# Performance work log

Measured on AMD Instinct MI355X. Metric: run time of the kernel, lower is better.

The kernel has to match this reference:

```python
import jax, jax.numpy as jnp
import numpy as np

B, IN, OUT = 4, 32, 64
N, NS = 163842, 40962  # icosahedron mesh levels: NS = (N + 6) / 4
EPS = 1e-5
SLOPE = 0.2


def setup_inputs() -> dict:
    key = jax.random.key(0)
    ks = jax.random.split(key, 8)
    x = jax.random.normal(ks[0], (B, IN, N), dtype=jnp.float32)
    x1 = jax.random.normal(ks[1], (B, OUT, NS), dtype=jnp.float32)
    pool_neigh = jax.random.randint(ks[2], (NS * 7,), 0, N, dtype=jnp.int32)
    neigh = jax.random.randint(ks[3], (NS * 7,), 0, NS, dtype=jnp.int32)
    W1 = jax.random.normal(ks[4], (OUT, 7 * IN), dtype=jnp.float32) / np.sqrt(7 * IN).astype(np.float32)
    b1 = jnp.zeros((OUT,), dtype=jnp.float32)
    gamma = jnp.ones((OUT,), dtype=jnp.float32)
    beta = jnp.zeros((OUT,), dtype=jnp.float32)
    Wc = jax.random.normal(ks[5], (OUT, 2 * OUT), dtype=jnp.float32) / np.sqrt(2 * OUT).astype(np.float32)
    bc = jnp.zeros((OUT,), dtype=jnp.float32)
    return dict(x=x, x1=x1, pool_neigh=pool_neigh, neigh=neigh,
                W1=W1, b1=b1, gamma=gamma, beta=beta, Wc=Wc, bc=bc)


def reference(x, x1, pool_neigh, neigh, W1, b1, gamma, beta, Wc, bc):
    b, c, n = x.shape
    ns = (n + 6) // 4
    # pool_layer_batch ('mean'): gather 7-neighborhood on fine mesh, mean-pool
    pooled = x[:, :, pool_neigh[: ns * 7]].reshape(b, c, ns, 7).mean(axis=3)  # [B, IN, NS]
    # onering_conv_layer_batch: gather 7-stencil, reshape to [B, NS, 7*IN], linear
    mat = pooled[:, :, neigh].reshape(b, c, ns, 7)          # [B, IN, NS, 7]
    mat = mat.transpose(0, 2, 3, 1).reshape(b, ns, 7 * c)   # [B, NS, 7*IN]
    h = jnp.einsum('bnk,ok->bon', mat, W1) + b1[None, :, None]  # [B, OUT, NS]
    # BatchNorm1d (track_running_stats=False -> always batch stats) + LeakyReLU(0.2)
    mu = h.mean(axis=(0, 2), keepdims=True)
    var = h.var(axis=(0, 2), keepdims=True)
    h = gamma[None, :, None] * (h - mu) * jax.lax.rsqrt(var + EPS) + beta[None, :, None]
    h = jnp.where(h >= 0, h, SLOPE * h)
    # concat skip + 1x1 Conv1d
    cat = jnp.concatenate([h, x1], axis=1)                  # [B, 2*OUT, NS]
    out = jnp.einsum('bcn,oc->bon', cat, Wc) + bc[None, :, None]
    return out
```

## Files before the change

### kernel.cpp

```cpp
#include <hip/hip_runtime.h>
#include <cstddef>

#define NB    4
#define CIN   32
#define COUT  64
#define NFINE 163842
#define NSV   40962
#define EPSB  1e-5f
#define SLOPE 0.2f

typedef __attribute__((ext_vector_type(8))) short short8;
typedef __attribute__((ext_vector_type(4))) float f32x4;

#define O_XT   ((size_t)0)
#define O_H    ((size_t)0)
#define O_X1T  ((size_t)22 << 20)
#define O_POOL ((size_t)48 << 20)
#define O_W1F  ((size_t)60 << 20)
#define O_WCF  ((size_t)60 << 20 | 0x8000)
#define O_ST   ((size_t)61 << 20)

static __device__ __forceinline__ short f2bf(float f) {
    union { float f; unsigned u; } v; v.f = f;
    unsigned r = v.u + 0x7fffu + ((v.u >> 16) & 1u);
    return (short)(r >> 16);
}
static __device__ __forceinline__ float bf2f(short h) {
    union { unsigned u; float f; } v;
    v.u = ((unsigned)(unsigned short)h) << 16;
    return v.f;
}

__global__ void k_prep(const float* __restrict__ W1, const float* __restrict__ Wc,
                       short* __restrict__ W1f, short* __restrict__ Wcf,
                       float* __restrict__ stats) {
    if (threadIdx.x < 128) stats[threadIdx.x] = 0.f;
    for (int i = threadIdx.x; i < 7 * 4 * 64 * 8; i += 256) {
        int e = i & 7, l = (i >> 3) & 63, nf = (i >> 9) & 3, kk = i >> 11;
        int o = 16 * nf + (l & 15);
        int k = 32 * kk + 8 * (l >> 4) + e;
        W1f[i] = f2bf(W1[o * (7 * CIN) + k]);
    }
    for (int i = threadIdx.x; i < 4 * 4 * 64 * 8; i += 256) {
        int e = i & 7, l = (i >> 3) & 63, nf = (i >> 9) & 3, kk = i >> 11;
        int o = 16 * nf + (l & 15);
        int c = 32 * kk + 8 * (l >> 4) + e;
        Wcf[i] = f2bf(Wc[o * (2 * COUT) + c]);
    }
}

__global__ __launch_bounds__(256) void k_transpose(
        const float* __restrict__ x, short* __restrict__ xt) {
    __shared__ float tile[128][33];
    const int n0 = blockIdx.x * 128;
    const int b  = blockIdx.y;
    const float* xb = x + (size_t)b * CIN * NFINE;
#pragma unroll
    for (int q = 0; q < 16; ++q) {
        int i = threadIdx.x + 256 * q;
        int c = i >> 7, nl = i & 127;
        int n = n0 + nl;
        tile[nl][c] = (n < NFINE) ? xb[(size_t)c * NFINE + n] : 0.f;
    }
    __syncthreads();
#pragma unroll
    for (int q = 0; q < 2; ++q) {
        int i = threadIdx.x + 256 * q;
        int nl = i >> 2, cg = i & 3;
        int n = n0 + nl;
        if (n >= NFINE) continue;
        short8 o;
#pragma unroll
        for (int e = 0; e < 8; ++e) o[e] = f2bf(tile[nl][8 * cg + e]);
        *(short8*)(xt + ((size_t)b * NFINE + n) * CIN + 8 * cg) = o;
    }
}

__global__ __launch_bounds__(256) void k_x1t(
        const float* __restrict__ x1, short* __restrict__ x1t) {
    __shared__ float tile[64][68];
    const int s0 = blockIdx.x * 64;
    const int b  = blockIdx.y;
    const float* xb = x1 + (size_t)b * COUT * NSV;
#pragma unroll
    for (int q = 0; q < 16; ++q) {
        int i = threadIdx.x + 256 * q;
        int c = i >> 6, sl = i & 63;
        int s = s0 + sl;
        tile[sl][c] = (s < NSV) ? xb[(size_t)c * NSV + s] : 0.f;
    }
    __syncthreads();
#pragma unroll
    for (int q = 0; q < 2; ++q) {
        int i = threadIdx.x + 256 * q;
        int sl = i >> 3, cg = i & 7;
        int s = s0 + sl;
        if (s >= NSV) continue;
        short8 o;
#pragma unroll
        for (int e = 0; e < 8; ++e) o[e] = f2bf(tile[sl][8 * cg + e]);
        *(short8*)(x1t + ((size_t)b * NSV + s) * COUT + 8 * cg) = o;
    }
}

__global__ __launch_bounds__(256) void k_pool(
        const short* __restrict__ xt, const int* __restrict__ pn,
        short* __restrict__ pooled) {
    const int s = blockIdx.x * 256 + threadIdx.x;
    const int b = blockIdx.y;
    if (s >= NSV) return;
    float acc[CIN];
#pragma unroll
    for (int c = 0; c < CIN; ++c) acc[c] = 0.f;
#pragma unroll
    for (int j = 0; j < 7; ++j) {
        const int t = pn[7 * s + j];
        const short8* vp = (const short8*)(xt + ((size_t)b * NFINE + t) * CIN);
#pragma unroll
        for (int g = 0; g < 4; ++g) {
            short8 v = vp[g];
#pragma unroll
            for (int e = 0; e < 8; ++e) acc[8 * g + e] += bf2f(v[e]);
        }
    }
    short* op = pooled + ((size_t)b * NSV + s) * CIN;
#pragma unroll
    for (int g = 0; g < 4; ++g) {
        short8 o;
#pragma unroll
        for (int e = 0; e < 8; ++e) o[e] = f2bf(acc[8 * g + e] * (1.f / 7.f));
        *(short8*)(op + 8 * g) = o;
    }
}

__global__ __launch_bounds__(256) void k_conv(
        const int* __restrict__ neigh, const short* __restrict__ W1f,
        const short* __restrict__ pooled, short* __restrict__ hbf,
        float* __restrict__ stats) {
    __shared__ float red[2][4][COUT];
    const int l = threadIdx.x & 63, w = threadIdx.x >> 6;
    const int b = blockIdx.y;
    const int s0 = blockIdx.x * 128 + w * 32;
    const int r = l & 15, g = l >> 4;

    f32x4 acc[2][4];
#pragma unroll
    for (int mf = 0; mf < 2; ++mf)
#pragma unroll
        for (int nf = 0; nf < 4; ++nf) acc[mf][nf] = (f32x4){0.f, 0.f, 0.f, 0.f};

    const short* pb = pooled + (size_t)b * NSV * CIN;
    const int sA0 = s0 + r, sA1 = s0 + 16 + r;
    const bool v0 = sA0 < NSV, v1 = sA1 < NSV;

#pragma unroll
    for (int kk = 0; kk < 7; ++kk) {
        const int t0 = v0 ? neigh[7 * sA0 + kk] : 0;
        const int t1 = v1 ? neigh[7 * sA1 + kk] : 0;
        short8 a0 = *(const short8*)(pb + (size_t)t0 * CIN + 8 * g);
        short8 a1 = *(const short8*)(pb + (size_t)t1 * CIN + 8 * g);
        const short8* wf = (const short8*)(W1f) + (size_t)kk * 4 * 64;
        short8 b0 = wf[0 * 64 + l];
        short8 b1 = wf[1 * 64 + l];
        short8 b2 = wf[2 * 64 + l];
        short8 b3 = wf[3 * 64 + l];
        acc[0][0] = __builtin_amdgcn_mfma_f32_16x16x32_bf16(a0, b0, acc[0][0], 0, 0, 0);
        acc[0][1] = __builtin_amdgcn_mfma_f32_16x16x32_bf16(a0, b1, acc[0][1], 0, 0, 0);
        acc[0][2] = __builtin_amdgcn_mfma_f32_16x16x32_bf16(a0, b2, acc[0][2], 0, 0, 0);
        acc[0][3] = __builtin_amdgcn_mfma_f32_16x16x32_bf16(a0, b3, acc[0][3], 0, 0, 0);
        acc[1][0] = __builtin_amdgcn_mfma_f32_16x16x32_bf16(a1, b0, acc[1][0], 0, 0, 0);
        acc[1][1] = __builtin_amdgcn_mfma_f32_16x16x32_bf16(a1, b1, acc[1][1], 0, 0, 0);
        acc[1][2] = __builtin_amdgcn_mfma_f32_16x16x32_bf16(a1, b2, acc[1][2], 0, 0, 0);
        acc[1][3] = __builtin_amdgcn_mfma_f32_16x16x32_bf16(a1, b3, acc[1][3], 0, 0, 0);
    }

    float sum[4], sq[4];
#pragma unroll
    for (int nf = 0; nf < 4; ++nf) { sum[nf] = 0.f; sq[nf] = 0.f; }
#pragma unroll
    for (int mf = 0; mf < 2; ++mf)
#pragma unroll
        for (int nf = 0; nf < 4; ++nf) {
            f32x4 d = acc[mf][nf];
#pragma unroll
            for (int rr = 0; rr < 4; ++rr) {
                const int srow = s0 + 16 * mf + 4 * g + rr;
                const float v = d[rr];
                const bool ok = srow < NSV;
                if (ok) hbf[((size_t)b * NSV + srow) * COUT + 16 * nf + r] = f2bf(v);
                const float vm = ok ? v : 0.f;
                sum[nf] += vm; sq[nf] += vm * vm;
            }
        }
#pragma unroll
    for (int nf = 0; nf < 4; ++nf) {
        float a = sum[nf], c = sq[nf];
        a += __shfl_xor(a, 16); a += __shfl_xor(a, 32);
        c += __shfl_xor(c, 16); c += __shfl_xor(c, 32);
        if (g == 0) { red[0][w][16 * nf + r] = a; red[1][w][16 * nf + r] = c; }
    }
    __syncthreads();
    if (threadIdx.x < COUT) {
        const int o = threadIdx.x;
        atomicAdd(&stats[o],        red[0][0][o] + red[0][1][o] + red[0][2][o] + red[0][3][o]);
        atomicAdd(&stats[COUT + o], red[1][0][o] + red[1][1][o] + red[1][2][o] + red[1][3][o]);
    }
}

__global__ void k_stats(const float* __restrict__ gamma,
                        const float* __restrict__ beta, float* __restrict__ st) {
    const int o = threadIdx.x;
    const float cnt = (float)((size_t)NB * NSV);
    float mu  = st[o] / cnt;
    float var = st[COUT + o] / cnt - mu * mu;
    float sc  = gamma[o] * rsqrtf(var + EPSB);
    st[2 * COUT + o] = sc;
    st[3 * COUT + o] = beta[o] - mu * sc;
}

__global__ __launch_bounds__(256) void k_out(
        const short* __restrict__ hbf, const short* __restrict__ x1t,
        const short* __restrict__ Wcf, const float* __restrict__ st,
        const float* __restrict__ bc, float* __restrict__ out) {
    __shared__ __attribute__((aligned(16))) short Wcs[4 * 4 * 64 * 8];
    __shared__ float scs[COUT], shs[COUT], bcs[COUT];
    {
        const short8* src = (const short8*)Wcf;
        short8* dst = (short8*)Wcs;
        for (int i = threadIdx.x; i < 1024; i += 256) dst[i] = src[i];
        if (threadIdx.x < COUT) {
            scs[threadIdx.x] = st[2 * COUT + threadIdx.x];
            shs[threadIdx.x] = st[3 * COUT + threadIdx.x];
            bcs[threadIdx.x] = bc[threadIdx.x];
        }
    }
    __syncthreads();

    const int l = threadIdx.x & 63, w = threadIdx.x >> 6;
    const int b = blockIdx.y;
    const int s0 = blockIdx.x * 128 + w * 32;
    const int r = l & 15, g = l >> 4;

    float scv[16], shv[16];
#pragma unroll
    for (int kk = 0; kk < 2; ++kk)
#pragma unroll
        for (int e = 0; e < 8; ++e) {
            scv[8 * kk + e] = scs[32 * kk + 8 * g + e];
            shv[8 * kk + e] = shs[32 * kk + 8 * g + e];
        }

    f32x4 acc[2][4];
#pragma unroll
    for (int mf = 0; mf < 2; ++mf)
#pragma unroll
        for (int nf = 0; nf < 4; ++nf) acc[mf][nf] = (f32x4){0.f, 0.f, 0.f, 0.f};

    int sa0 = s0 + r;       if (sa0 > NSV - 1) sa0 = NSV - 1;
    int sa1 = s0 + 16 + r;  if (sa1 > NSV - 1) sa1 = NSV - 1;
    const size_t rowA0 = ((size_t)b * NSV + sa0) * COUT;
    const size_t rowA1 = ((size_t)b * NSV + sa1) * COUT;

#pragma unroll
    for (int kk = 0; kk < 4; ++kk) {
        short8 a0, a1;
        if (kk < 2) {
            short8 h0 = *(const short8*)(hbf + rowA0 + 32 * kk + 8 * g);
            short8 h1 = *(const short8*)(hbf + rowA1 + 32 * kk + 8 * g);
#pragma unroll
            for (int e = 0; e < 8; ++e) {
                float z0 = scv[8 * kk + e] * bf2f(h0[e]) + shv[8 * kk + e];
                float z1 = scv[8 * kk + e] * bf2f(h1[e]) + shv[8 * kk + e];
                z0 = fmaxf(z0, SLOPE * z0);
                z1 = fmaxf(z1, SLOPE * z1);
                a0[e] = f2bf(z0); a1[e] = f2bf(z1);
            }
        } else {
            a0 = *(const short8*)(x1t + rowA0 + 32 * (kk - 2) + 8 * g);
            a1 = *(const short8*)(x1t + rowA1 + 32 * (kk - 2) + 8 * g);
        }
        const short8* wf = (const short8*)Wcs + kk * 4 * 64;
#pragma unroll
        for (int nf = 0; nf < 4; ++nf) {
            short8 bfv = wf[nf * 64 + l];
            acc[0][nf] = __builtin_amdgcn_mfma_f32_16x16x32_bf16(a0, bfv, acc[0][nf], 0, 0, 0);
            acc[1][nf] = __builtin_amdgcn_mfma_f32_16x16x32_bf16(a1, bfv, acc[1][nf], 0, 0, 0);
        }
    }

    float* ob = out + (size_t)b * COUT * NSV;
#pragma unroll
    for (int mf = 0; mf < 2; ++mf)
#pragma unroll
        for (int nf = 0; nf < 4; ++nf) {
            const int o  = 16 * nf + r;
            const int sr = s0 + 16 * mf + 4 * g;
            f32x4 d = acc[mf][nf];
            const float bb = bcs[o];
            float* p = ob + (size_t)o * NSV + sr;
            if (sr + 3 < NSV) {
                *(float2*)(p)     = make_float2(d[0] + bb, d[1] + bb);
                *(float2*)(p + 2) = make_float2(d[2] + bb, d[3] + bb);
            } else {
#pragma unroll
                for (int rr = 0; rr < 4; ++rr)
                    if (sr + rr < NSV) p[rr] = d[rr] + bb;
            }
        }
}

extern "C" void kernel_launch(void* const* d_in, const int* in_sizes, int n_in,
                              void* d_out, int out_size, void* d_ws, size_t ws_size,
                              hipStream_t stream) {
    const float* x          = (const float*)d_in[0];
    const float* x1         = (const float*)d_in[1];
    const int*   pool_neigh = (const int*)d_in[2];
    const int*   neigh      = (const int*)d_in[3];
    const float* W1         = (const float*)d_in[4];
    const float* gamma      = (const float*)d_in[6];
    const float* beta       = (const float*)d_in[7];
    const float* Wc         = (const float*)d_in[8];
    const float* bc         = (const float*)d_in[9];

    char* wsb = (char*)d_ws;
    short* xt     = (short*)(wsb + O_XT);
    short* hbf    = (short*)(wsb + O_H);
    short* x1t    = (short*)(wsb + O_X1T);
    short* pooled = (short*)(wsb + O_POOL);
    short* W1f    = (short*)(wsb + O_W1F);
    short* Wcf    = (short*)(wsb + O_WCF);
    float* stats  = (float*)(wsb + O_ST);
    float* out    = (float*)d_out;

    k_prep<<<1, 256, 0, stream>>>(W1, Wc, W1f, Wcf, stats);
    k_transpose<<<dim3((NFINE + 127) / 128, NB), 256, 0, stream>>>(x, xt);
    k_pool<<<dim3((NSV + 255) / 256, NB), 256, 0, stream>>>(xt, pool_neigh, pooled);
    k_x1t<<<dim3((NSV + 63) / 64, NB), 256, 0, stream>>>(x1, x1t);
    k_conv<<<dim3((NSV + 127) / 128, NB), 256, 0, stream>>>(neigh, W1f, pooled, hbf, stats);
    k_stats<<<1, 64, 0, stream>>>(gamma, beta, stats);
    k_out<<<dim3((NSV + 127) / 128, NB), 256, 0, stream>>>(hbf, x1t, Wcf, stats, bc, out);
}
```

Before: 328.2 us.

## Fuse x1 transpose into output kernel and batch gather loads in pool/conv

Removes the separate x1 transpose kernel. The output kernel now reads x1 directly in its channel-major fp32 layout and converts it to bf16 in registers, which saves one write and one read of a transposed intermediate plus a launch. The pool and conv kernels now issue all seven neighbour gathers before accumulating, so more memory requests are in flight at once. The direct x1 reads are strided per lane (coalesced across lanes along s), and the prefetched gathers raise register pressure.

Measured after the change: 342.9 us. 4.5% more time.

```diff
diff --git a/kernel.cpp b/kernel.cpp
--- a/kernel.cpp
+++ b/kernel.cpp
@@ -14,7 +14,6 @@
 
 #define O_XT   ((size_t)0)
 #define O_H    ((size_t)0)
-#define O_X1T  ((size_t)22 << 20)
 #define O_POOL ((size_t)48 << 20)
 #define O_W1F  ((size_t)60 << 20)
 #define O_WCF  ((size_t)60 << 20 | 0x8000)
@@ -76,60 +75,34 @@
     }
 }
 
-__global__ __launch_bounds__(256) void k_x1t(
-        const float* __restrict__ x1, short* __restrict__ x1t) {
-    __shared__ float tile[64][68];
-    const int s0 = blockIdx.x * 64;
-    const int b  = blockIdx.y;
-    const float* xb = x1 + (size_t)b * COUT * NSV;
-#pragma unroll
-    for (int q = 0; q < 16; ++q) {
-        int i = threadIdx.x + 256 * q;
-        int c = i >> 6, sl = i & 63;
-        int s = s0 + sl;
-        tile[sl][c] = (s < NSV) ? xb[(size_t)c * NSV + s] : 0.f;
-    }
-    __syncthreads();
-#pragma unroll
-    for (int q = 0; q < 2; ++q) {
-        int i = threadIdx.x + 256 * q;
-        int sl = i >> 3, cg = i & 7;
-        int s = s0 + sl;
-        if (s >= NSV) continue;
-        short8 o;
-#pragma unroll
-        for (int e = 0; e < 8; ++e) o[e] = f2bf(tile[sl][8 * cg + e]);
-        *(short8*)(x1t + ((size_t)b * NSV + s) * COUT + 8 * cg) = o;
-    }
-}
-
 __global__ __launch_bounds__(256) void k_pool(
         const short* __restrict__ xt, const int* __restrict__ pn,
         short* __restrict__ pooled) {
     const int s = blockIdx.x * 256 + threadIdx.x;
     const int b = blockIdx.y;
     if (s >= NSV) return;
-    float acc[CIN];
-#pragma unroll
-    for (int c = 0; c < CIN; ++c) acc[c] = 0.f;
-#pragma unroll
-    for (int j = 0; j < 7; ++j) {
-        const int t = pn[7 * s + j];
-        const short8* vp = (const short8*)(xt + ((size_t)b * NFINE + t) * CIN);
-#pragma unroll
-        for (int g = 0; g < 4; ++g) {
-            short8 v = vp[g];
-#pragma unroll
-            for (int e = 0; e < 8; ++e) acc[8 * g + e] += bf2f(v[e]);
-        }
-    }
+    int t[7];
+#pragma unroll
+    for (int j = 0; j < 7; ++j) t[j] = pn[7 * s + j];
+    const short* xb = xt + (size_t)b * NFINE * CIN;
     short* op = pooled + ((size_t)b * NSV + s) * CIN;
 #pragma unroll
-    for (int g = 0; g < 4; ++g) {
+    for (int gq = 0; gq < 4; ++gq) {
+        short8 v[7];
+#pragma unroll
+        for (int j = 0; j < 7; ++j)
+            v[j] = *(const short8*)(xb + (size_t)t[j] * CIN + 8 * gq);
+        float a8[8];
+#pragma unroll
+        for (int e = 0; e < 8; ++e) a8[e] = 0.f;
+#pragma unroll
+        for (int j = 0; j < 7; ++j)
+#pragma unroll
+            for (int e = 0; e < 8; ++e) a8[e] += bf2f(v[j][e]);
         short8 o;
 #pragma unroll
-        for (int e = 0; e < 8; ++e) o[e] = f2bf(acc[8 * g + e] * (1.f / 7.f));
-        *(short8*)(op + 8 * g) = o;
+        for (int e = 0; e < 8; ++e) o[e] = f2bf(a8[e] * (1.f / 7.f));
+        *(short8*)(op + 8 * gq) = o;
     }
 }
 
@@ -143,35 +116,37 @@
     const int s0 = blockIdx.x * 128 + w * 32;
     const int r = l & 15, g = l >> 4;
 
-    f32x4 acc[2][4];
-#pragma unroll
-    for (int mf = 0; mf < 2; ++mf)
-#pragma unroll
-        for (int nf = 0; nf < 4; ++nf) acc[mf][nf] = (f32x4){0.f, 0.f, 0.f, 0.f};
-
     const short* pb = pooled + (size_t)b * NSV * CIN;
     const int sA0 = s0 + r, sA1 = s0 + 16 + r;
     const bool v0 = sA0 < NSV, v1 = sA1 < NSV;
-
+    const int c0 = v0 ? sA0 : NSV - 1, c1 = v1 ? sA1 : NSV - 1;
+
+    int t0[7], t1[7];
+#pragma unroll
+    for (int kk = 0; kk < 7; ++kk) { t0[kk] = neigh[7 * c0 + kk]; t1[kk] = neigh[7 * c1 + kk]; }
+
+    short8 a0[7], a1[7];
 #pragma unroll
     for (int kk = 0; kk < 7; ++kk) {
-        const int t0 = v0 ? neigh[7 * sA0 + kk] : 0;
-        const int t1 = v1 ? neigh[7 * sA1 + kk] : 0;
-        short8 a0 = *(const short8*)(pb + (size_t)t0 * CIN + 8 * g);
-        short8 a1 = *(const short8*)(pb + (size_t)t1 * CIN + 8 * g);
-        const short8* wf = (const short8*)(W1f) + (size_t)kk * 4 * 64;
-        short8 b0 = wf[0 * 64 + l];
-        short8 b1 = wf[1 * 64 + l];
-        short8 b2 = wf[2 * 64 + l];
-        short8 b3 = wf[3 * 64 + l];
-        acc[0][0] = __builtin_amdgcn_mfma_f32_16x16x32_bf16(a0, b0, acc[0][0], 0, 0, 0);
-        acc[0][1] = __builtin_amdgcn_mfma_f32_16x16x32_bf16(a0, b1, acc[0][1], 0, 0, 0);
-        acc[0][2] = __builtin_amdgcn_mfma_f32_16x16x32_bf16(a0, b2, acc[0][2], 0, 0, 0);
-        acc[0][3] = __builtin_amdgcn_mfma_f32_16x16x32_bf16(a0, b3, acc[0][3], 0, 0, 0);
-        acc[1][0] = __builtin_amdgcn_mfma_f32_16x16x32_bf16(a1, b0, acc[1][0], 0, 0, 0);
-        acc[1][1] = __builtin_amdgcn_mfma_f32_16x16x32_bf16(a1, b1, acc[1][1], 0, 0, 0);
-        acc[1][2] = __builtin_amdgcn_mfma_f32_16x16x32_bf16(a1, b2, acc[1][2], 0, 0, 0);
-        acc[1][3] = __builtin_amdgcn_mfma_f32_16x16x32_bf16(a1, b3, acc[1][3], 0, 0, 0);
+        a0[kk] = *(const short8*)(pb + (size_t)t0[kk] * CIN + 8 * g);
+        a1[kk] = *(const short8*)(pb + (size_t)t1[kk] * CIN + 8 * g);
+    }
+
+    f32x4 acc[2][4];
+#pragma unroll
+    for (int mf = 0; mf < 2; ++mf)
+#pragma unroll
+        for (int nf = 0; nf < 4; ++nf) acc[mf][nf] = (f32x4){0.f, 0.f, 0.f, 0.f};
+
+#pragma unroll
+    for (int kk = 0; kk < 7; ++kk) {
+        const short8* wf = (const short8*)(W1f) + (size_t)kk * 256;
+#pragma unroll
+        for (int nf = 0; nf < 4; ++nf) {
+            short8 bfv = wf[nf * 64 + l];
+            acc[0][nf] = __builtin_amdgcn_mfma_f32_16x16x32_bf16(a0[kk], bfv, acc[0][nf], 0, 0, 0);
+            acc[1][nf] = __builtin_amdgcn_mfma_f32_16x16x32_bf16(a1[kk], bfv, acc[1][nf], 0, 0, 0);
+        }
     }
 
     float sum[4], sq[4];
@@ -219,7 +194,7 @@
 }
 
 __global__ __launch_bounds__(256) void k_out(
-        const short* __restrict__ hbf, const short* __restrict__ x1t,
+        const short* __restrict__ hbf, const float* __restrict__ x1,
         const short* __restrict__ Wcf, const float* __restrict__ st,
         const float* __restrict__ bc, float* __restrict__ out) {
     __shared__ __attribute__((aligned(16))) short Wcs[4 * 4 * 64 * 8];
@@ -241,43 +216,59 @@
     const int s0 = blockIdx.x * 128 + w * 32;
     const int r = l & 15, g = l >> 4;
 
-    float scv[16], shv[16];
-#pragma unroll
-    for (int kk = 0; kk < 2; ++kk)
-#pragma unroll
-        for (int e = 0; e < 8; ++e) {
-            scv[8 * kk + e] = scs[32 * kk + 8 * g + e];
-            shv[8 * kk + e] = shs[32 * kk + 8 * g + e];
-        }
-
-    f32x4 acc[2][4];
-#pragma unroll
-    for (int mf = 0; mf < 2; ++mf)
-#pragma unroll
-        for (int nf = 0; nf < 4; ++nf) acc[mf][nf] = (f32x4){0.f, 0.f, 0.f, 0.f};
-
     int sa0 = s0 + r;       if (sa0 > NSV - 1) sa0 = NSV - 1;
     int sa1 = s0 + 16 + r;  if (sa1 > NSV - 1) sa1 = NSV - 1;
     const size_t rowA0 = ((size_t)b * NSV + sa0) * COUT;
     const size_t rowA1 = ((size_t)b * NSV + sa1) * COUT;
 
+    short8 h00 = *(const short8*)(hbf + rowA0 + 8 * g);
+    short8 h01 = *(const short8*)(hbf + rowA0 + 32 + 8 * g);
+    short8 h10 = *(const short8*)(hbf + rowA1 + 8 * g);
+    short8 h11 = *(const short8*)(hbf + rowA1 + 32 + 8 * g);
+    const float* x1b = x1 + (size_t)b * COUT * NSV;
+    float xv0[16], xv1[16];
+#pragma unroll
+    for (int i = 0; i < 16; ++i) {
+        const int c2 = 32 * (i >> 3) + 8 * g + (i & 7);
+        xv0[i] = x1b[(size_t)c2 * NSV + sa0];
+        xv1[i] = x1b[(size_t)c2 * NSV + sa1];
+    }
+
+    float scv[16], shv[16];
+#pragma unroll
+    for (int kk = 0; kk < 2; ++kk)
+#pragma unroll
+        for (int e = 0; e < 8; ++e) {
+            scv[8 * kk + e] = scs[32 * kk + 8 * g + e];
+            shv[8 * kk + e] = shs[32 * kk + 8 * g + e];
+        }
+
+    f32x4 acc[2][4];
+#pragma unroll
+    for (int mf = 0; mf < 2; ++mf)
+#pragma unroll
+        for (int nf = 0; nf < 4; ++nf) acc[mf][nf] = (f32x4){0.f, 0.f, 0.f, 0.f};
+
 #pragma unroll
     for (int kk = 0; kk < 4; ++kk) {
         short8 a0, a1;
         if (kk < 2) {
-            short8 h0 = *(const short8*)(hbf + rowA0 + 32 * kk + 8 * g);
-            short8 h1 = *(const short8*)(hbf + rowA1 + 32 * kk + 8 * g);
+            short8 hh0 = kk ? h01 : h00;
+            short8 hh1 = kk ? h11 : h10;
 #pragma unroll
             for (int e = 0; e < 8; ++e) {
-                float z0 = scv[8 * kk + e] * bf2f(h0[e]) + shv[8 * kk + e];
-                float z1 = scv[8 * kk + e] * bf2f(h1[e]) + shv[8 * kk + e];
+                float z0 = scv[8 * kk + e] * bf2f(hh0[e]) + shv[8 * kk + e];
+                float z1 = scv[8 * kk + e] * bf2f(hh1[e]) + shv[8 * kk + e];
                 z0 = fmaxf(z0, SLOPE * z0);
                 z1 = fmaxf(z1, SLOPE * z1);
                 a0[e] = f2bf(z0); a1[e] = f2bf(z1);
             }
         } else {
-            a0 = *(const short8*)(x1t + rowA0 + 32 * (kk - 2) + 8 * g);
-            a1 = *(const short8*)(x1t + rowA1 + 32 * (kk - 2) + 8 * g);
+#pragma unroll
+            for (int e = 0; e < 8; ++e) {
+                a0[e] = f2bf(xv0[8 * (kk - 2) + e]);
+                a1[e] = f2bf(xv1[8 * (kk - 2) + e]);
+            }
         }
         const short8* wf = (const short8*)Wcs + kk * 4 * 64;
 #pragma unroll
@@ -325,7 +316,6 @@
     char* wsb = (char*)d_ws;
     short* xt     = (short*)(wsb + O_XT);
     short* hbf    = (short*)(wsb + O_H);
-    short* x1t    = (short*)(wsb + O_X1T);
     short* pooled = (short*)(wsb + O_POOL);
     short* W1f    = (short*)(wsb + O_W1F);
     short* Wcf    = (short*)(wsb + O_WCF);
@@ -335,8 +325,7 @@
     k_prep<<<1, 256, 0, stream>>>(W1, Wc, W1f, Wcf, stats);
     k_transpose<<<dim3((NFINE + 127) / 128, NB), 256, 0, stream>>>(x, xt);
     k_pool<<<dim3((NSV + 255) / 256, NB), 256, 0, stream>>>(xt, pool_neigh, pooled);
-    k_x1t<<<dim3((NSV + 63) / 64, NB), 256, 0, stream>>>(x1, x1t);
     k_conv<<<dim3((NSV + 127) / 128, NB), 256, 0, stream>>>(neigh, W1f, pooled, hbf, stats);
     k_stats<<<1, 64, 0, stream>>>(gamma, beta, stats);
-    k_out<<<dim3((NSV + 127) / 128, NB), 256, 0, stream>>>(hbf, x1t, Wcf, stats, bc, out);
-}
+    k_out<<<dim3((NSV + 127) / 128, NB), 256, 0, stream>>>(hbf, x1, Wcf, stats, bc, out);
+}
```
